# Kernel tuning notes

Hardware: AMD Instinct MI355X
Metric: run time of the kernel (lower is better)

## Reference

```python
import jax, jax.numpy as jnp
import numpy as np

D_MODEL = 2048
N_HEADS = 16
HEAD_DIM = D_MODEL // N_HEADS
ROPE_BASE = 10000.0
B, T = 2, 2048


def setup_inputs() -> dict:
    key = jax.random.key(0)
    k1, k2, k3 = jax.random.split(key, 3)
    s_in = 1.0 / np.sqrt(D_MODEL)
    x = jax.random.normal(k1, (B, T, D_MODEL), dtype=jnp.float32)
    Wqkv = jax.random.normal(k2, (3 * D_MODEL, D_MODEL), dtype=jnp.float32) * s_in
    bqkv = jnp.zeros((3 * D_MODEL,), dtype=jnp.float32)
    Wo = jax.random.normal(k3, (D_MODEL, D_MODEL), dtype=jnp.float32) * s_in
    bo = jnp.zeros((D_MODEL,), dtype=jnp.float32)
    return {"x": x, "Wqkv": Wqkv, "bqkv": bqkv, "Wo": Wo, "bo": bo}


def _rotate_half(x):
    # [x1,x2,x3,x4] -> [-x2,x1,-x4,x3] (interleaved pairs)
    x_even = x[..., 0::2]
    x_odd = x[..., 1::2]
    return jnp.stack((-x_odd, x_even), axis=-1).reshape(x.shape)


def _rope_cos_sin(seq_len, dtype):
    half = HEAD_DIM // 2
    inv_freq = 1.0 / (ROPE_BASE ** (jnp.arange(half, dtype=jnp.float32) / half))
    freqs = jnp.arange(seq_len, dtype=jnp.float32)[:, None] * inv_freq[None, :]  # (T, half)
    emb = jnp.repeat(freqs, 2, axis=-1)  # (T, D) interleaved
    cos = jnp.cos(emb).astype(dtype)[None, None]  # (1,1,T,D)
    sin = jnp.sin(emb).astype(dtype)[None, None]
    return cos, sin


def reference(x, Wqkv, bqkv, Wo, bo):
    b, t, c = x.shape
    qkv = jnp.einsum('btc,fc->btf', x, Wqkv) + bqkv  # (B,T,3C)
    q, k, v = jnp.split(qkv, 3, axis=-1)
    def to_heads(z):
        return z.reshape(b, t, N_HEADS, HEAD_DIM).transpose(0, 2, 1, 3)  # (B,H,T,D)
    q, k, v = to_heads(q), to_heads(k), to_heads(v)
    cos, sin = _rope_cos_sin(t, x.dtype)
    q = q * cos + _rotate_half(q) * sin
    k = k * cos + _rotate_half(k) * sin
    scale = 1.0 / jnp.sqrt(jnp.asarray(HEAD_DIM, dtype=x.dtype))
    scores = jnp.einsum('bhqd,bhkd->bhqk', q, k) * scale  # (B,H,T,T)
    causal = jnp.tril(jnp.ones((t, t), dtype=bool))
    scores = jnp.where(causal, scores, jnp.finfo(scores.dtype).min)
    attn = jax.nn.softmax(scores, axis=-1)
    out = jnp.einsum('bhqk,bhkd->bhqd', attn, v)  # (B,H,T,D)
    out = out.transpose(0, 2, 1, 3).reshape(b, t, c)
    return jnp.einsum('btc,oc->bto', out, Wo) + bo
```

## Files before the change

kernel.cpp:

```cpp
#include <hip/hip_runtime.h>

using f16 = _Float16;
typedef _Float16 h8 __attribute__((ext_vector_type(8)));
typedef _Float16 h4 __attribute__((ext_vector_type(4)));
typedef float f4 __attribute__((ext_vector_type(4)));
typedef unsigned int u32;
typedef unsigned long long u64;

#define DEVI static __device__ __forceinline__

DEVI f4 mfma16(h8 a, h8 b, f4 c) {
  return __builtin_amdgcn_mfma_f32_16x16x32_f16(a, b, c, 0, 0, 0);
}

DEVI void gl_lds16(const f16* g, f16* l) {
  __builtin_amdgcn_global_load_lds(
      (const __attribute__((address_space(1))) u32*)g,
      (__attribute__((address_space(3))) u32*)l, 16, 0, 0);
}

DEVI u32 pkh2(float a, float b) {
  union { f16 h[2]; u32 u; } x;
  x.h[0] = (f16)a; x.h[1] = (f16)b;
  return x.u;
}

typedef float fv4 __attribute__((ext_vector_type(4)));

__global__ __launch_bounds__(256) void k_cvt(const float* __restrict__ in,
                                             f16* __restrict__ out, int n4) {
  int i = blockIdx.x * 256 + threadIdx.x;
  if (i >= n4) return;
  fv4 v = ((const fv4*)in)[i];
  h4 o;
  o[0] = (f16)v[0]; o[1] = (f16)v[1]; o[2] = (f16)v[2]; o[3] = (f16)v[3];
  ((h4*)out)[i] = o;
}

__global__ __launch_bounds__(256) void k_rope_tbl(float* __restrict__ tbl) {
  int i = blockIdx.x * 256 + threadIdx.x;
  int t = i >> 6, d = i & 63;
  float invf = exp2f(-(float)d * (13.287712379549449f / 64.f));
  float a = (float)t * invf;
  tbl[2 * i]     = cosf(a);
  tbl[2 * i + 1] = sinf(a);
}

template <int F32OUT>
__global__ __launch_bounds__(512, 2) void k_gemm256(const f16* __restrict__ A,
                                                    const f16* __restrict__ Bt,
                                                    const float* __restrict__ bias,
                                                    void* __restrict__ Cp,
                                                    int M, int N, int K, int gy) {
  __shared__ f16 lds[2][24576];
  const int tid = threadIdx.x;
  const int w = tid >> 6, lane = tid & 63;
  const int g = lane >> 4, colq = lane & 15;
  const int wr = w >> 2, wc = w & 3;

  const int nwg = gridDim.x;
  const int q8 = nwg >> 3;
  const int swz = (blockIdx.x & 7) * q8 + (blockIdx.x >> 3);
  const int bm = swz % gy, bn = swz / gy;

  const f16* Ab = A + (size_t)bm * 128 * K;
  const f16* Bb = Bt + (size_t)bn * 256 * K;

  const int srow = lane >> 3;
  const int schunk = (lane & 7) ^ srow;
  const int nt = K >> 6;

  auto STAGE = [&](int kt, f16* buf) {
    const int k0 = kt << 6;
    f16* bA = buf;
    f16* bB = buf + 128 * 64;
#pragma unroll
    for (int j = 0; j < 2; ++j) {
      const int r = w * 16 + j * 8;
      gl_lds16(Ab + (size_t)(r + srow) * K + k0 + schunk * 8, bA + r * 64);
    }
#pragma unroll
    for (int j = 0; j < 4; ++j) {
      const int r = w * 32 + j * 8;
      gl_lds16(Bb + (size_t)(r + srow) * K + k0 + schunk * 8, bB + r * 64);
    }
  };

  STAGE(0, lds[0]);
  STAGE(1, lds[1]);
  asm volatile("s_waitcnt vmcnt(6)" ::: "memory");
  __builtin_amdgcn_s_barrier();

  f4 acc[4][4] = {};
  const int rowA0 = wr * 64 + colq;
  const int rowB0 = wc * 64 + colq;
  const int cq7 = colq & 7;

  for (int t = 0; t < nt; ++t) {
    f16* cur = lds[t & 1];
    h8 af[2][4], bf[2][4];
#pragma unroll
    for (int kki = 0; kki < 2; ++kki) {
#pragma unroll
      for (int m = 0; m < 4; ++m)
        af[kki][m] = *(const h8*)(cur + (rowA0 + m * 16) * 64 + (((kki * 4 + g) ^ cq7) * 8));
#pragma unroll
      for (int n = 0; n < 4; ++n)
        bf[kki][n] = *(const h8*)(cur + 8192 + (rowB0 + n * 16) * 64 + (((kki * 4 + g) ^ cq7) * 8));
    }
    asm volatile("s_waitcnt lgkmcnt(0)" ::: "memory");
    __builtin_amdgcn_s_barrier();
    const bool more = (t + 2 < nt);
    if (more) STAGE(t + 2, cur);
    __builtin_amdgcn_s_setprio(1);
#pragma unroll
    for (int m = 0; m < 4; ++m)
#pragma unroll
      for (int n = 0; n < 4; ++n)
#pragma unroll
        for (int kki = 0; kki < 2; ++kki)
          acc[m][n] = mfma16(af[kki][m], bf[kki][n], acc[m][n]);
    __builtin_amdgcn_s_setprio(0);
    if (more) {
      asm volatile("s_waitcnt vmcnt(6)" ::: "memory");
    } else {
      asm volatile("s_waitcnt vmcnt(0)" ::: "memory");
    }
    __builtin_amdgcn_s_barrier();
  }

#pragma unroll
  for (int n = 0; n < 4; ++n) {
    const int col = bn * 256 + wc * 64 + n * 16 + colq;
    const float bv = bias[col];
#pragma unroll
    for (int m = 0; m < 4; ++m) {
      const int row0 = bm * 128 + wr * 64 + m * 16 + 4 * g;
#pragma unroll
      for (int r = 0; r < 4; ++r) {
        float v = acc[m][n][r] + bv;
        if constexpr (F32OUT) {
          ((float*)Cp)[(size_t)(row0 + r) * N + col] = v;
        } else {
          ((f16*)Cp)[(size_t)(row0 + r) * N + col] = (f16)v;
        }
      }
    }
  }
}

__global__ __launch_bounds__(256) void k_rope(const f16* __restrict__ qkv,
                                              const float* __restrict__ tbl,
                                              f16* __restrict__ Q, f16* __restrict__ K) {
  int i = blockIdx.x * 256 + threadIdx.x;
  int d = i & 63;
  int h = (i >> 6) & 15;
  int bt = i >> 10;
  int t = bt & 2047;
  int bh = ((bt >> 11) << 4) | h;
  union { u32 u; f16 h2[2]; } qa, ka, qo, ko;
  qa.u = *(const u32*)(qkv + (size_t)bt * 6144 + h * 128 + 2 * d);
  ka.u = *(const u32*)(qkv + (size_t)bt * 6144 + 2048 + h * 128 + 2 * d);
  float c = tbl[2 * (t * 64 + d)];
  float s = tbl[2 * (t * 64 + d) + 1];
  float q0f = (float)qa.h2[0], q1f = (float)qa.h2[1];
  float k0f = (float)ka.h2[0], k1f = (float)ka.h2[1];
  const float SQ = 0.088388347648318447f * 1.4426950408889634f;
  qo.h2[0] = (f16)((q0f * c - q1f * s) * SQ);
  qo.h2[1] = (f16)((q1f * c + q0f * s) * SQ);
  ko.h2[0] = (f16)(k0f * c - k1f * s);
  ko.h2[1] = (f16)(k1f * c + k0f * s);
  *(u32*)(Q + ((size_t)bh * 2048 + t) * 128 + 2 * d) = qo.u;
  *(u32*)(K + ((size_t)bh * 2048 + t) * 128 + 2 * d) = ko.u;
}

__global__ __launch_bounds__(256) void k_vtrans(const f16* __restrict__ qkv,
                                                f16* __restrict__ Vt) {
  __shared__ f16 ldsT[128 * 40];
  const int bh = blockIdx.y, t0 = blockIdx.x * 32;
  const int b = bh >> 4, h = bh & 15;
  const int tid = threadIdx.x;
#pragma unroll
  for (int cc = 0; cc < 2; ++cc) {
    int task = tid + cc * 256;
    int row = task >> 4;
    int ch = task & 15;
    h8 v = *(const h8*)(qkv + (size_t)(b * 2048 + t0 + row) * 6144 + 4096 + h * 128 + ch * 8);
#pragma unroll
    for (int j = 0; j < 8; ++j) ldsT[(ch * 8 + j) * 40 + row] = v[j];
  }
  __syncthreads();
  int d = tid >> 1, seg = tid & 1;
  h8 v0 = *(const h8*)(ldsT + d * 40 + seg * 16);
  h8 v1 = *(const h8*)(ldsT + d * 40 + seg * 16 + 8);
  f16* dst = Vt + ((size_t)bh * 128 + d) * 2048 + t0 + seg * 16;
  *(h8*)dst = v0;
  *(h8*)(dst + 8) = v1;
}

DEVI void stage_tiles(const f16* __restrict__ Kg, const f16* __restrict__ Vtg,
                      f16* bufK, f16* bufV, int kv, int w, int lane) {
#pragma unroll
  for (int jj = 0; jj < 4; ++jj) {
    const int j = w * 4 + jj;
    const int rK = j * 4 + (lane >> 4);
    const int cK = (lane & 15) ^ ((rK & 7) << 1);
    gl_lds16(Kg + (size_t)(kv + rK) * 128 + cK * 8, bufK + j * 512);
    const int rV = j * 8 + (lane >> 3);
    const int cV = (lane & 7) ^ (rV & 7);
    gl_lds16(Vtg + (size_t)rV * 2048 + kv + cV * 8, bufV + j * 512);
  }
}

__global__ __launch_bounds__(256, 1) void k_attn(const f16* __restrict__ Q,
                                                 const f16* __restrict__ K,
                                                 const f16* __restrict__ Vt,
                                                 f16* __restrict__ O) {
  __shared__ f16 lds[2][16384];
  const int tid = threadIdx.x;
  const int w = tid >> 6, lane = tid & 63;
  const int g = lane >> 4, q = lane & 15;
  const int bid = blockIdx.x;
  const int bh = bid & 31;
  const int b = bid >> 5;

  const f16* Kg = K + (size_t)bh * 2048 * 128;
  const f16* Vtg = Vt + (size_t)bh * 128 * 2048;
  const int qx2 = (q & 7) << 1;
  const int qx = q & 7;

  for (int ph = 0; ph < 2; ++ph) {
    const int p = ph ? (15 - b) : b;
    const int q0w = p * 128 + w * 32;
    const int nit = 2 * (p + 1);

    h8 qf[2][4];
#pragma unroll
    for (int set = 0; set < 2; ++set)
#pragma unroll
      for (int d4 = 0; d4 < 4; ++d4)
        qf[set][d4] = *(const h8*)(Q + ((size_t)bh * 2048 + q0w + 16 * set + q) * 128 + d4 * 32 + g * 8);

    stage_tiles(Kg, Vtg, lds[0], lds[0] + 8192, 0, w, lane);
    asm volatile("s_waitcnt vmcnt(0)" ::: "memory");
    __builtin_amdgcn_s_barrier();

    f4 ot[2][8] = {};
    float mrun[2] = {-3.0e38f, -3.0e38f};
    float lrun[2] = {0.f, 0.f};

    for (int it = 0; it < nit; ++it) {
      const int kv0 = it * 64;
      f16* bufK = lds[it & 1];
      f16* bufV = bufK + 8192;
      if (it + 1 < nit) {
        f16* nb = lds[(it + 1) & 1];
        stage_tiles(Kg, Vtg, nb, nb + 8192, kv0 + 64, w, lane);
      }
      if (kv0 < q0w + 32) {
        f4 st[2][4] = {{{0.f,0.f,0.f,0.f},{0.f,0.f,0.f,0.f},{0.f,0.f,0.f,0.f},{0.f,0.f,0.f,0.f}},
                       {{0.f,0.f,0.f,0.f},{0.f,0.f,0.f,0.f},{0.f,0.f,0.f,0.f},{0.f,0.f,0.f,0.f}}};
#pragma unroll
        for (int d4 = 0; d4 < 4; ++d4) {
          h8 kf[4];
#pragma unroll
          for (int s = 0; s < 4; ++s)
            kf[s] = *(const h8*)(bufK + ((16 * s + q) * 16 + ((4 * d4 + g) ^ qx2)) * 8);
#pragma unroll
          for (int set = 0; set < 2; ++set)
#pragma unroll
            for (int s = 0; s < 4; ++s)
              st[set][s] = mfma16(kf[s], qf[set][d4], st[set][s]);
        }
        if (kv0 + 63 > q0w) {
#pragma unroll
          for (int set = 0; set < 2; ++set) {
            const int qcol = q0w + 16 * set + q;
#pragma unroll
            for (int s = 0; s < 4; ++s)
#pragma unroll
              for (int r = 0; r < 4; ++r)
                if (kv0 + s * 16 + 4 * g + r > qcol) st[set][s][r] = -3.0e38f;
          }
        }
        float pm[2];
#pragma unroll
        for (int set = 0; set < 2; ++set) {
          float m0 = st[set][0][0];
#pragma unroll
          for (int s = 0; s < 4; ++s)
#pragma unroll
            for (int r = 0; r < 4; ++r) m0 = fmaxf(m0, st[set][s][r]);
          m0 = fmaxf(m0, __shfl_xor(m0, 16));
          m0 = fmaxf(m0, __shfl_xor(m0, 32));
          pm[set] = m0;
        }
        const bool ok = (pm[0] <= mrun[0] + 8.0f) && (pm[1] <= mrun[1] + 8.0f);
        if (!__all(ok)) {
#pragma unroll
          for (int set = 0; set < 2; ++set) {
            float mnew = fmaxf(mrun[set], pm[set]);
            float corr = exp2f(mrun[set] - mnew);
            lrun[set] *= corr;
#pragma unroll
            for (int dt = 0; dt < 8; ++dt) ot[set][dt] *= corr;
            mrun[set] = mnew;
          }
        }
#pragma unroll
        for (int set = 0; set < 2; ++set) {
          float ps = 0.f;
#pragma unroll
          for (int s = 0; s < 4; ++s)
#pragma unroll
            for (int r = 0; r < 4; ++r) {
              st[set][s][r] = exp2f(st[set][s][r] - mrun[set]);
              ps += st[set][s][r];
            }
          ps += __shfl_xor(ps, 16);
          ps += __shfl_xor(ps, 32);
          lrun[set] += ps;
        }
        union { u32 u[4]; h8 h; } pb[2][2];
        const int s0l = ((g & 1) << 5) | q;
        const bool hi = g >= 2;
#pragma unroll
        for (int set = 0; set < 2; ++set)
#pragma unroll
          for (int hh = 0; hh < 2; ++hh) {
            u32 wA0 = pkh2(st[set][2 * hh][0], st[set][2 * hh][1]);
            u32 wB0 = pkh2(st[set][2 * hh][2], st[set][2 * hh][3]);
            u32 wA1 = pkh2(st[set][2 * hh + 1][0], st[set][2 * hh + 1][1]);
            u32 wB1 = pkh2(st[set][2 * hh + 1][2], st[set][2 * hh + 1][3]);
            u32 a0 = (u32)__shfl((int)wA0, s0l),      a1 = (u32)__shfl((int)wA1, s0l);
            u32 b0 = (u32)__shfl((int)wB0, s0l),      b1 = (u32)__shfl((int)wB1, s0l);
            u32 c0 = (u32)__shfl((int)wA0, s0l + 16), c1 = (u32)__shfl((int)wA1, s0l + 16);
            u32 d0 = (u32)__shfl((int)wB0, s0l + 16), d1 = (u32)__shfl((int)wB1, s0l + 16);
            pb[set][hh].u[0] = hi ? a1 : a0;
            pb[set][hh].u[1] = hi ? b1 : b0;
            pb[set][hh].u[2] = hi ? c1 : c0;
            pb[set][hh].u[3] = hi ? d1 : d0;
          }
#pragma unroll
        for (int hh = 0; hh < 2; ++hh)
#pragma unroll
          for (int dt = 0; dt < 8; ++dt) {
            h8 vf = *(const h8*)(bufV + ((dt * 16 + q) * 8 + ((4 * hh + g) ^ qx)) * 8);
#pragma unroll
            for (int set = 0; set < 2; ++set)
              ot[set][dt] = mfma16(vf, pb[set][hh].h, ot[set][dt]);
          }
      }
      asm volatile("s_waitcnt vmcnt(0)" ::: "memory");
      __builtin_amdgcn_s_barrier();
    }

#pragma unroll
    for (int set = 0; set < 2; ++set) {
      float linv = 1.0f / lrun[set];
      f16* Ob = O + ((size_t)(bh >> 4) * 2048 + q0w + 16 * set + q) * 2048 + (bh & 15) * 128 + 4 * g;
#pragma unroll
      for (int dt = 0; dt < 8; ++dt) {
        union { f16 hh4[4]; u64 u; } o;
#pragma unroll
        for (int r = 0; r < 4; ++r) o.hh4[r] = (f16)(ot[set][dt][r] * linv);
        *(u64*)(Ob + dt * 16) = o.u;
      }
    }
  }
}

extern "C" void kernel_launch(void* const* d_in, const int* in_sizes, int n_in,
                              void* d_out, int out_size, void* d_ws, size_t ws_size,
                              hipStream_t stream) {
  (void)in_sizes; (void)n_in; (void)out_size; (void)ws_size;
  const float* x    = (const float*)d_in[0];
  const float* Wqkv = (const float*)d_in[1];
  const float* bqkv = (const float*)d_in[2];
  const float* Wo   = (const float*)d_in[3];
  const float* bo   = (const float*)d_in[4];

  char* ws = (char*)d_ws;
  f16* xb    = (f16*)ws; ws += (size_t)4096 * 2048 * 2;
  f16* wqkvb = (f16*)ws; ws += (size_t)6144 * 2048 * 2;
  f16* wob   = (f16*)ws; ws += (size_t)2048 * 2048 * 2;
  f16* qkvb  = (f16*)ws; ws += (size_t)4096 * 6144 * 2;
  f16* Qb    = (f16*)ws; ws += (size_t)32 * 2048 * 128 * 2;
  f16* Kb    = (f16*)ws; ws += (size_t)32 * 2048 * 128 * 2;
  f16* Vtb   = (f16*)ws; ws += (size_t)32 * 128 * 2048 * 2;
  f16* attb  = (f16*)ws; ws += (size_t)4096 * 2048 * 2;
  float* tbl = (float*)ws; ws += (size_t)2048 * 64 * 2 * 4;

  k_cvt<<<8192, 256, 0, stream>>>(x, xb, 2097152);
  k_cvt<<<12288, 256, 0, stream>>>(Wqkv, wqkvb, 3145728);
  k_cvt<<<4096, 256, 0, stream>>>(Wo, wob, 1048576);
  k_rope_tbl<<<512, 256, 0, stream>>>(tbl);

  k_gemm256<0><<<768, 512, 0, stream>>>(xb, wqkvb, bqkv, qkvb, 4096, 6144, 2048, 32);

  k_rope<<<16384, 256, 0, stream>>>(qkvb, tbl, Qb, Kb);
  k_vtrans<<<dim3(64, 32), 256, 0, stream>>>(qkvb, Vtb);

  k_attn<<<256, 256, 0, stream>>>(Qb, Kb, Vtb, attb);

  k_gemm256<1><<<256, 512, 0, stream>>>(attb, wob, bo, d_out, 4096, 2048, 2048, 32);
}
```

Baseline: 317.9 us.

## Fuse RoPE into QKV GEMM epilogue and split attention into one block per tile

Adds a new 128x128-tile QKV GEMM that applies bias, RoPE and the softmax scale in its epilogue and writes Q and K directly in head-major layout, which removes the separate rope kernel and its round trip through the qkv buffer. The attention kernel now launches 512 blocks, each handling a single query tile instead of a pair of tiles, which gives more parallelism at the cost of less balanced per-block work. The new GEMM is single-buffered with a barrier every K step and scatters 2-byte stores, so it may be slower than the previous 256-wide double-buffered GEMM. The old GEMM template is renamed and still used for the output projection.

Result: no change. 313.8 us (-1.3%).

```diff
diff --git a/kernel.cpp b/kernel.cpp
--- a/kernel.cpp
+++ b/kernel.cpp
@@ -46,8 +46,115 @@
   tbl[2 * i + 1] = sinf(a);
 }
 
+__global__ __launch_bounds__(256) void k_gemm_qkv(const f16* __restrict__ A,
+                                                  const f16* __restrict__ Bt,
+                                                  const float* __restrict__ bias,
+                                                  const float* __restrict__ tbl,
+                                                  f16* __restrict__ Qb,
+                                                  f16* __restrict__ Kb,
+                                                  f16* __restrict__ qkvb,
+                                                  int K) {
+  __shared__ f16 sA[128 * 64];
+  __shared__ f16 sB[128 * 64];
+  const int tid = threadIdx.x;
+  const int w = tid >> 6, lane = tid & 63;
+  const int g = lane >> 4, colq = lane & 15;
+  const int wr = w >> 1, wc = w & 1;
+
+  const int nwg = gridDim.x;
+  const int q8 = nwg >> 3;
+  const int swz = (blockIdx.x & 7) * q8 + (blockIdx.x >> 3);
+  const int bm = swz & 31, bn = swz >> 5;
+
+  const f16* Ab = A + (size_t)bm * 128 * K;
+  const f16* Bb = Bt + (size_t)bn * 128 * K;
+  const int nt = K >> 6;
+
+  const int srow = lane >> 3;
+  const int schunk = (lane & 7) ^ srow;
+  const int cq7 = colq & 7;
+
+  f4 acc[4][4] = {};
+  const int rowA0 = wr * 64 + colq;
+  const int rowB0 = wc * 64 + colq;
+
+  for (int t = 0; t < nt; ++t) {
+    const int k0 = t << 6;
+#pragma unroll
+    for (int j = 0; j < 4; ++j) {
+      const int r = (w * 4 + j) * 8;
+      gl_lds16(Ab + (size_t)(r + srow) * K + k0 + schunk * 8, sA + r * 64);
+      gl_lds16(Bb + (size_t)(r + srow) * K + k0 + schunk * 8, sB + r * 64);
+    }
+    __syncthreads();
+    h8 af[2][4], bf[2][4];
+#pragma unroll
+    for (int kki = 0; kki < 2; ++kki) {
+#pragma unroll
+      for (int m = 0; m < 4; ++m)
+        af[kki][m] = *(const h8*)(sA + (rowA0 + m * 16) * 64 + (((kki * 4 + g) ^ cq7) * 8));
+#pragma unroll
+      for (int n = 0; n < 4; ++n)
+        bf[kki][n] = *(const h8*)(sB + (rowB0 + n * 16) * 64 + (((kki * 4 + g) ^ cq7) * 8));
+    }
+#pragma unroll
+    for (int m = 0; m < 4; ++m)
+#pragma unroll
+      for (int n = 0; n < 4; ++n)
+#pragma unroll
+        for (int kki = 0; kki < 2; ++kki)
+          acc[m][n] = mfma16(af[kki][m], bf[kki][n], acc[m][n]);
+    __syncthreads();
+  }
+
+  const int sect = bn >> 4;
+  const int h = bn & 15;
+  if (sect == 2) {
+#pragma unroll
+    for (int n = 0; n < 4; ++n) {
+      const int col = bn * 128 + wc * 64 + n * 16 + colq;
+      const float bv = bias[col];
+#pragma unroll
+      for (int m = 0; m < 4; ++m) {
+        const int row0 = bm * 128 + wr * 64 + m * 16 + 4 * g;
+#pragma unroll
+        for (int r = 0; r < 4; ++r)
+          qkvb[(size_t)(row0 + r) * 6144 + col] = (f16)(acc[m][n][r] + bv);
+      }
+    }
+  } else {
+    f16* Out = sect ? Kb : Qb;
+    const float SQ = 0.088388347648318447f * 1.4426950408889634f;
+    const float scale = sect ? 1.0f : SQ;
+    const float2* tbl2 = (const float2*)tbl;
+#pragma unroll
+    for (int n = 0; n < 4; ++n) {
+      const int col = bn * 128 + wc * 64 + n * 16 + colq;
+      const int d = col & 127;
+      const int dd = d >> 1;
+      const bool odd = (d & 1) != 0;
+      const float bv = bias[col];
+#pragma unroll
+      for (int m = 0; m < 4; ++m) {
+        const int row0 = bm * 128 + wr * 64 + m * 16 + 4 * g;
+#pragma unroll
+        for (int r = 0; r < 4; ++r) {
+          const int row = row0 + r;
+          const int t = row & 2047;
+          const int b = row >> 11;
+          float v = acc[m][n][r] + bv;
+          float p = __shfl_xor(v, 1);
+          float2 cs = tbl2[t * 64 + dd];
+          float o = odd ? (v * cs.x + p * cs.y) : (v * cs.x - p * cs.y);
+          Out[((size_t)(b * 16 + h) * 2048 + t) * 128 + d] = (f16)(o * scale);
+        }
+      }
+    }
+  }
+}
+
 template <int F32OUT>
-__global__ __launch_bounds__(512, 2) void k_gemm256(const f16* __restrict__ A,
+__global__ __launch_bounds__(512, 2) void k_gemm128(const f16* __restrict__ A,
                                                     const f16* __restrict__ Bt,
                                                     const float* __restrict__ bias,
                                                     void* __restrict__ Cp,
@@ -149,31 +256,6 @@
   }
 }
 
-__global__ __launch_bounds__(256) void k_rope(const f16* __restrict__ qkv,
-                                              const float* __restrict__ tbl,
-                                              f16* __restrict__ Q, f16* __restrict__ K) {
-  int i = blockIdx.x * 256 + threadIdx.x;
-  int d = i & 63;
-  int h = (i >> 6) & 15;
-  int bt = i >> 10;
-  int t = bt & 2047;
-  int bh = ((bt >> 11) << 4) | h;
-  union { u32 u; f16 h2[2]; } qa, ka, qo, ko;
-  qa.u = *(const u32*)(qkv + (size_t)bt * 6144 + h * 128 + 2 * d);
-  ka.u = *(const u32*)(qkv + (size_t)bt * 6144 + 2048 + h * 128 + 2 * d);
-  float c = tbl[2 * (t * 64 + d)];
-  float s = tbl[2 * (t * 64 + d) + 1];
-  float q0f = (float)qa.h2[0], q1f = (float)qa.h2[1];
-  float k0f = (float)ka.h2[0], k1f = (float)ka.h2[1];
-  const float SQ = 0.088388347648318447f * 1.4426950408889634f;
-  qo.h2[0] = (f16)((q0f * c - q1f * s) * SQ);
-  qo.h2[1] = (f16)((q1f * c + q0f * s) * SQ);
-  ko.h2[0] = (f16)(k0f * c - k1f * s);
-  ko.h2[1] = (f16)(k1f * c + k0f * s);
-  *(u32*)(Q + ((size_t)bh * 2048 + t) * 128 + 2 * d) = qo.u;
-  *(u32*)(K + ((size_t)bh * 2048 + t) * 128 + 2 * d) = ko.u;
-}
-
 __global__ __launch_bounds__(256) void k_vtrans(const f16* __restrict__ qkv,
                                                 f16* __restrict__ Vt) {
   __shared__ f16 ldsT[128 * 40];
@@ -212,160 +294,157 @@
   }
 }
 
-__global__ __launch_bounds__(256, 1) void k_attn(const f16* __restrict__ Q,
-                                                 const f16* __restrict__ K,
-                                                 const f16* __restrict__ Vt,
-                                                 f16* __restrict__ O) {
+__global__ __launch_bounds__(256) void k_attn(const f16* __restrict__ Q,
+                                              const f16* __restrict__ K,
+                                              const f16* __restrict__ Vt,
+                                              f16* __restrict__ O) {
   __shared__ f16 lds[2][16384];
   const int tid = threadIdx.x;
   const int w = tid >> 6, lane = tid & 63;
   const int g = lane >> 4, q = lane & 15;
   const int bid = blockIdx.x;
   const int bh = bid & 31;
-  const int b = bid >> 5;
+  const int p = (bid < 256) ? (bid >> 5) : (15 - ((bid - 256) >> 5));
 
   const f16* Kg = K + (size_t)bh * 2048 * 128;
   const f16* Vtg = Vt + (size_t)bh * 128 * 2048;
   const int qx2 = (q & 7) << 1;
   const int qx = q & 7;
 
-  for (int ph = 0; ph < 2; ++ph) {
-    const int p = ph ? (15 - b) : b;
-    const int q0w = p * 128 + w * 32;
-    const int nit = 2 * (p + 1);
-
-    h8 qf[2][4];
-#pragma unroll
-    for (int set = 0; set < 2; ++set)
-#pragma unroll
-      for (int d4 = 0; d4 < 4; ++d4)
-        qf[set][d4] = *(const h8*)(Q + ((size_t)bh * 2048 + q0w + 16 * set + q) * 128 + d4 * 32 + g * 8);
-
-    stage_tiles(Kg, Vtg, lds[0], lds[0] + 8192, 0, w, lane);
+  const int q0w = p * 128 + w * 32;
+  const int nit = 2 * (p + 1);
+
+  h8 qf[2][4];
+#pragma unroll
+  for (int set = 0; set < 2; ++set)
+#pragma unroll
+    for (int d4 = 0; d4 < 4; ++d4)
+      qf[set][d4] = *(const h8*)(Q + ((size_t)bh * 2048 + q0w + 16 * set + q) * 128 + d4 * 32 + g * 8);
+
+  stage_tiles(Kg, Vtg, lds[0], lds[0] + 8192, 0, w, lane);
+  asm volatile("s_waitcnt vmcnt(0)" ::: "memory");
+  __builtin_amdgcn_s_barrier();
+
+  f4 ot[2][8] = {};
+  float mrun[2] = {-3.0e38f, -3.0e38f};
+  float lrun[2] = {0.f, 0.f};
+
+  for (int it = 0; it < nit; ++it) {
+    const int kv0 = it * 64;
+    f16* bufK = lds[it & 1];
+    f16* bufV = bufK + 8192;
+    if (it + 1 < nit) {
+      f16* nb = lds[(it + 1) & 1];
+      stage_tiles(Kg, Vtg, nb, nb + 8192, kv0 + 64, w, lane);
+    }
+    if (kv0 < q0w + 32) {
+      f4 st[2][4] = {{{0.f,0.f,0.f,0.f},{0.f,0.f,0.f,0.f},{0.f,0.f,0.f,0.f},{0.f,0.f,0.f,0.f}},
+                     {{0.f,0.f,0.f,0.f},{0.f,0.f,0.f,0.f},{0.f,0.f,0.f,0.f},{0.f,0.f,0.f,0.f}}};
+#pragma unroll
+      for (int d4 = 0; d4 < 4; ++d4) {
+        h8 kf[4];
+#pragma unroll
+        for (int s = 0; s < 4; ++s)
+          kf[s] = *(const h8*)(bufK + ((16 * s + q) * 16 + ((4 * d4 + g) ^ qx2)) * 8);
+#pragma unroll
+        for (int set = 0; set < 2; ++set)
+#pragma unroll
+          for (int s = 0; s < 4; ++s)
+            st[set][s] = mfma16(kf[s], qf[set][d4], st[set][s]);
+      }
+      if (kv0 + 63 > q0w) {
+#pragma unroll
+        for (int set = 0; set < 2; ++set) {
+          const int qcol = q0w + 16 * set + q;
+#pragma unroll
+          for (int s = 0; s < 4; ++s)
+#pragma unroll
+            for (int r = 0; r < 4; ++r)
+              if (kv0 + s * 16 + 4 * g + r > qcol) st[set][s][r] = -3.0e38f;
+        }
+      }
+      float pm[2];
+#pragma unroll
+      for (int set = 0; set < 2; ++set) {
+        float m0 = st[set][0][0];
+#pragma unroll
+        for (int s = 0; s < 4; ++s)
+#pragma unroll
+          for (int r = 0; r < 4; ++r) m0 = fmaxf(m0, st[set][s][r]);
+        m0 = fmaxf(m0, __shfl_xor(m0, 16));
+        m0 = fmaxf(m0, __shfl_xor(m0, 32));
+        pm[set] = m0;
+      }
+      const bool ok = (pm[0] <= mrun[0] + 8.0f) && (pm[1] <= mrun[1] + 8.0f);
+      if (!__all(ok)) {
+#pragma unroll
+        for (int set = 0; set < 2; ++set) {
+          float mnew = fmaxf(mrun[set], pm[set]);
+          float corr = exp2f(mrun[set] - mnew);
+          lrun[set] *= corr;
+#pragma unroll
+          for (int dt = 0; dt < 8; ++dt) ot[set][dt] *= corr;
+          mrun[set] = mnew;
+        }
+      }
+#pragma unroll
+      for (int set = 0; set < 2; ++set) {
+        float ps = 0.f;
+#pragma unroll
+        for (int s = 0; s < 4; ++s)
+#pragma unroll
+          for (int r = 0; r < 4; ++r) {
+            st[set][s][r] = exp2f(st[set][s][r] - mrun[set]);
+            ps += st[set][s][r];
+          }
+        ps += __shfl_xor(ps, 16);
+        ps += __shfl_xor(ps, 32);
+        lrun[set] += ps;
+      }
+      union { u32 u[4]; h8 h; } pb[2][2];
+      const int s0l = ((g & 1) << 5) | q;
+      const bool hi = g >= 2;
+#pragma unroll
+      for (int set = 0; set < 2; ++set)
+#pragma unroll
+        for (int hh = 0; hh < 2; ++hh) {
+          u32 wA0 = pkh2(st[set][2 * hh][0], st[set][2 * hh][1]);
+          u32 wB0 = pkh2(st[set][2 * hh][2], st[set][2 * hh][3]);
+          u32 wA1 = pkh2(st[set][2 * hh + 1][0], st[set][2 * hh + 1][1]);
+          u32 wB1 = pkh2(st[set][2 * hh + 1][2], st[set][2 * hh + 1][3]);
+          u32 a0 = (u32)__shfl((int)wA0, s0l),      a1 = (u32)__shfl((int)wA1, s0l);
+          u32 b0 = (u32)__shfl((int)wB0, s0l),      b1 = (u32)__shfl((int)wB1, s0l);
+          u32 c0 = (u32)__shfl((int)wA0, s0l + 16), c1 = (u32)__shfl((int)wA1, s0l + 16);
+          u32 d0 = (u32)__shfl((int)wB0, s0l + 16), d1 = (u32)__shfl((int)wB1, s0l + 16);
+          pb[set][hh].u[0] = hi ? a1 : a0;
+          pb[set][hh].u[1] = hi ? b1 : b0;
+          pb[set][hh].u[2] = hi ? c1 : c0;
+          pb[set][hh].u[3] = hi ? d1 : d0;
+        }
+#pragma unroll
+      for (int hh = 0; hh < 2; ++hh)
+#pragma unroll
+        for (int dt = 0; dt < 8; ++dt) {
+          h8 vf = *(const h8*)(bufV + ((dt * 16 + q) * 8 + ((4 * hh + g) ^ qx)) * 8);
+#pragma unroll
+          for (int set = 0; set < 2; ++set)
+            ot[set][dt] = mfma16(vf, pb[set][hh].h, ot[set][dt]);
+        }
+    }
     asm volatile("s_waitcnt vmcnt(0)" ::: "memory");
     __builtin_amdgcn_s_barrier();
-
-    f4 ot[2][8] = {};
-    float mrun[2] = {-3.0e38f, -3.0e38f};
-    float lrun[2] = {0.f, 0.f};
-
-    for (int it = 0; it < nit; ++it) {
-      const int kv0 = it * 64;
-      f16* bufK = lds[it & 1];
-      f16* bufV = bufK + 8192;
-      if (it + 1 < nit) {
-        f16* nb = lds[(it + 1) & 1];
-        stage_tiles(Kg, Vtg, nb, nb + 8192, kv0 + 64, w, lane);
-      }
-      if (kv0 < q0w + 32) {
-        f4 st[2][4] = {{{0.f,0.f,0.f,0.f},{0.f,0.f,0.f,0.f},{0.f,0.f,0.f,0.f},{0.f,0.f,0.f,0.f}},
-                       {{0.f,0.f,0.f,0.f},{0.f,0.f,0.f,0.f},{0.f,0.f,0.f,0.f},{0.f,0.f,0.f,0.f}}};
-#pragma unroll
-        for (int d4 = 0; d4 < 4; ++d4) {
-          h8 kf[4];
-#pragma unroll
-          for (int s = 0; s < 4; ++s)
-            kf[s] = *(const h8*)(bufK + ((16 * s + q) * 16 + ((4 * d4 + g) ^ qx2)) * 8);
-#pragma unroll
-          for (int set = 0; set < 2; ++set)
-#pragma unroll
-            for (int s = 0; s < 4; ++s)
-              st[set][s] = mfma16(kf[s], qf[set][d4], st[set][s]);
-        }
-        if (kv0 + 63 > q0w) {
-#pragma unroll
-          for (int set = 0; set < 2; ++set) {
-            const int qcol = q0w + 16 * set + q;
-#pragma unroll
-            for (int s = 0; s < 4; ++s)
-#pragma unroll
-              for (int r = 0; r < 4; ++r)
-                if (kv0 + s * 16 + 4 * g + r > qcol) st[set][s][r] = -3.0e38f;
-          }
-        }
-        float pm[2];
-#pragma unroll
-        for (int set = 0; set < 2; ++set) {
-          float m0 = st[set][0][0];
-#pragma unroll
-          for (int s = 0; s < 4; ++s)
-#pragma unroll
-            for (int r = 0; r < 4; ++r) m0 = fmaxf(m0, st[set][s][r]);
-          m0 = fmaxf(m0, __shfl_xor(m0, 16));
-          m0 = fmaxf(m0, __shfl_xor(m0, 32));
-          pm[set] = m0;
-        }
-        const bool ok = (pm[0] <= mrun[0] + 8.0f) && (pm[1] <= mrun[1] + 8.0f);
-        if (!__all(ok)) {
-#pragma unroll
-          for (int set = 0; set < 2; ++set) {
-            float mnew = fmaxf(mrun[set], pm[set]);
-            float corr = exp2f(mrun[set] - mnew);
-            lrun[set] *= corr;
-#pragma unroll
-            for (int dt = 0; dt < 8; ++dt) ot[set][dt] *= corr;
-            mrun[set] = mnew;
-          }
-        }
-#pragma unroll
-        for (int set = 0; set < 2; ++set) {
-          float ps = 0.f;
-#pragma unroll
-          for (int s = 0; s < 4; ++s)
-#pragma unroll
-            for (int r = 0; r < 4; ++r) {
-              st[set][s][r] = exp2f(st[set][s][r] - mrun[set]);
-              ps += st[set][s][r];
-            }
-          ps += __shfl_xor(ps, 16);
-          ps += __shfl_xor(ps, 32);
-          lrun[set] += ps;
-        }
-        union { u32 u[4]; h8 h; } pb[2][2];
-        const int s0l = ((g & 1) << 5) | q;
-        const bool hi = g >= 2;
-#pragma unroll
-        for (int set = 0; set < 2; ++set)
-#pragma unroll
-          for (int hh = 0; hh < 2; ++hh) {
-            u32 wA0 = pkh2(st[set][2 * hh][0], st[set][2 * hh][1]);
-            u32 wB0 = pkh2(st[set][2 * hh][2], st[set][2 * hh][3]);
-            u32 wA1 = pkh2(st[set][2 * hh + 1][0], st[set][2 * hh + 1][1]);
-            u32 wB1 = pkh2(st[set][2 * hh + 1][2], st[set][2 * hh + 1][3]);
-            u32 a0 = (u32)__shfl((int)wA0, s0l),      a1 = (u32)__shfl((int)wA1, s0l);
-            u32 b0 = (u32)__shfl((int)wB0, s0l),      b1 = (u32)__shfl((int)wB1, s0l);
-            u32 c0 = (u32)__shfl((int)wA0, s0l + 16), c1 = (u32)__shfl((int)wA1, s0l + 16);
-            u32 d0 = (u32)__shfl((int)wB0, s0l + 16), d1 = (u32)__shfl((int)wB1, s0l + 16);
-            pb[set][hh].u[0] = hi ? a1 : a0;
-            pb[set][hh].u[1] = hi ? b1 : b0;
-            pb[set][hh].u[2] = hi ? c1 : c0;
-            pb[set][hh].u[3] = hi ? d1 : d0;
-          }
-#pragma unroll
-        for (int hh = 0; hh < 2; ++hh)
-#pragma unroll
-          for (int dt = 0; dt < 8; ++dt) {
-            h8 vf = *(const h8*)(bufV + ((dt * 16 + q) * 8 + ((4 * hh + g) ^ qx)) * 8);
-#pragma unroll
-            for (int set = 0; set < 2; ++set)
-              ot[set][dt] = mfma16(vf, pb[set][hh].h, ot[set][dt]);
-          }
-      }
-      asm volatile("s_waitcnt vmcnt(0)" ::: "memory");
-      __builtin_amdgcn_s_barrier();
-    }
-
-#pragma unroll
-    for (int set = 0; set < 2; ++set) {
-      float linv = 1.0f / lrun[set];
-      f16* Ob = O + ((size_t)(bh >> 4) * 2048 + q0w + 16 * set + q) * 2048 + (bh & 15) * 128 + 4 * g;
-#pragma unroll
-      for (int dt = 0; dt < 8; ++dt) {
-        union { f16 hh4[4]; u64 u; } o;
-#pragma unroll
-        for (int r = 0; r < 4; ++r) o.hh4[r] = (f16)(ot[set][dt][r] * linv);
-        *(u64*)(Ob + dt * 16) = o.u;
-      }
+  }
+
+#pragma unroll
+  for (int set = 0; set < 2; ++set) {
+    float linv = 1.0f / lrun[set];
+    f16* Ob = O + ((size_t)(bh >> 4) * 2048 + q0w + 16 * set + q) * 2048 + (bh & 15) * 128 + 4 * g;
+#pragma unroll
+    for (int dt = 0; dt < 8; ++dt) {
+      union { f16 hh4[4]; u64 u; } o;
+#pragma unroll
+      for (int r = 0; r < 4; ++r) o.hh4[r] = (f16)(ot[set][dt][r] * linv);
+      *(u64*)(Ob + dt * 16) = o.u;
     }
   }
 }
@@ -396,12 +475,11 @@
   k_cvt<<<4096, 256, 0, stream>>>(Wo, wob, 1048576);
   k_rope_tbl<<<512, 256, 0, stream>>>(tbl);
 
-  k_gemm256<0><<<768, 512, 0, stream>>>(xb, wqkvb, bqkv, qkvb, 4096, 6144, 2048, 32);
-
-  k_rope<<<16384, 256, 0, stream>>>(qkvb, tbl, Qb, Kb);
+  k_gemm_qkv<<<1536, 256, 0, stream>>>(xb, wqkvb, bqkv, tbl, Qb, Kb, qkvb, 2048);
+
   k_vtrans<<<dim3(64, 32), 256, 0, stream>>>(qkvb, Vtb);
 
-  k_attn<<<256, 256, 0, stream>>>(Qb, Kb, Vtb, attb);
-
-  k_gemm256<1><<<256, 512, 0, stream>>>(attb, wob, bo, d_out, 4096, 2048, 2048, 32);
-}
+  k_attn<<<512, 256, 0, stream>>>(Qb, Kb, Vtb, attb);
+
+  k_gemm128<1><<<256, 512, 0, stream>>>(attb, wob, bo, d_out, 4096, 2048, 2048, 32);
+}
```
